# Optimization experiments

Measured on AMD Instinct MI355X. Metric: run time of the kernel, lower is better.

## Reference

```python
import jax, jax.numpy as jnp
import numpy as np

B, C, H, W = 2, 64, 128, 128
KH = KW = 3
K = KH * KW
PAD = 1


def conv(x, w, b, pad):
    out = jax.lax.conv_general_dilated(
        x, w, window_strides=(1, 1), padding=[(pad, pad), (pad, pad)],
        dimension_numbers=("NCHW", "OIHW", "NCHW"))
    return out + b[None, :, None, None]


def leaky_relu(x, slope=0.2):
    return jnp.where(x >= 0, x, slope * x)


def deform_conv(img, offset, mask, w, b):
    # img: [B,C,Hi,Wi]; offset: [B,2K,H,W] (dy,dx interleaved per tap); mask: [B,K,H,W]
    Bb, Ci, Hi, Wi = img.shape
    Ho, Wo = offset.shape[2], offset.shape[3]
    off = offset.reshape(Bb, K, 2, Ho, Wo)
    dy, dx = off[:, :, 0], off[:, :, 1]
    ki, kj = jnp.meshgrid(jnp.arange(KH), jnp.arange(KW), indexing="ij")
    ki = ki.reshape(K).astype(img.dtype)
    kj = kj.reshape(K).astype(img.dtype)
    base_h = (jnp.arange(Ho) - PAD).astype(img.dtype)
    base_w = (jnp.arange(Wo) - PAD).astype(img.dtype)
    ys = base_h[None, None, :, None] + ki[None, :, None, None] + dy  # [B,K,Ho,Wo]
    xs = base_w[None, None, None, :] + kj[None, :, None, None] + dx

    y0 = jnp.floor(ys)
    x0 = jnp.floor(xs)
    ty = ys - y0
    tx = xs - x0
    y0i = y0.astype(jnp.int32)
    x0i = x0.astype(jnp.int32)
    flat = img.reshape(Bb, Ci, Hi * Wi)

    def corner(yi, xi, wgt):
        valid = (yi >= 0) & (yi < Hi) & (xi >= 0) & (xi < Wi)
        yc = jnp.clip(yi, 0, Hi - 1)
        xc = jnp.clip(xi, 0, Wi - 1)
        idx = (yc * Wi + xc).reshape(Bb, 1, -1)
        v = jnp.take_along_axis(flat, jnp.broadcast_to(idx, (Bb, Ci, idx.shape[-1])), axis=2)
        v = v.reshape(Bb, Ci, K, Ho, Wo)
        return v * (wgt * valid.astype(img.dtype))[:, None]

    samp = (corner(y0i, x0i, (1 - ty) * (1 - tx))
            + corner(y0i, x0i + 1, (1 - ty) * tx)
            + corner(y0i + 1, x0i, ty * (1 - tx))
            + corner(y0i + 1, x0i + 1, ty * tx))  # [B,C,K,Ho,Wo]
    out = jnp.einsum("ock,bckhw->bohw", w.reshape(w.shape[0], Ci, K), samp * mask[:, None])
    return out + b[None, :, None, None]


def setup_inputs() -> dict:
    key = jax.random.key(0)
    ks = jax.random.split(key, 8)
    s = 0.05  # keep predicted offsets in a realistic few-pixel range
    return {
        "x": jax.random.normal(ks[0], (B, C, H, W), jnp.float32),
        "y": jax.random.normal(ks[1], (B, C, H, W), jnp.float32),
        "w0": jax.random.normal(ks[2], (C, C, 1, 1), jnp.float32) * s,
        "b0": jnp.zeros((C,), jnp.float32),
        "w_om": jax.random.normal(ks[3], (3 * K, 2 * C, KH, KW), jnp.float32) * s,
        "b_om": jnp.zeros((3 * K,), jnp.float32),
        "w_dc": jax.random.normal(ks[4], (C, C, KH, KW), jnp.float32) * s,
        "b_dc": jnp.zeros((C,), jnp.float32),
        "w1": jax.random.normal(ks[5], (C, C, KH, KW), jnp.float32) * s,
        "b1": jnp.zeros((C,), jnp.float32),
        "w2": jax.random.normal(ks[6], (C, C, KH, KW), jnp.float32) * s,
        "b2": jnp.zeros((C,), jnp.float32),
    }


def reference(x, y, w0, b0, w_om, b_om, w_dc, b_dc, w1, b1, w2, b2):
    x0 = conv(x, w0, b0, pad=0)  # 1x1 projection
    om = conv(jnp.concatenate([x0, y], axis=1), w_om, b_om, pad=PAD)
    offset = om[:, : 2 * K]
    mask = 2.0 * jax.nn.sigmoid(om[:, 2 * K :])
    out = x0 + deform_conv(y, offset, mask, w_dc, b_dc)
    return conv(leaky_relu(conv(out, w1, b1, pad=PAD)), w2, b2, pad=PAD) + out
```

## Files before the change

kernel.cpp:

```cpp
#include <hip/hip_runtime.h>
#include <hip/hip_bf16.h>
#include <math.h>

#define BB 2
#define CCH 64
#define HH 128
#define WWD 128
#define HWv (HH*WWD)
#define KK 9
#define KSTEP 18
#define OMKS 36
#define TCOLS 34
#define CSTR 72
#define CSTR2 136
#define DROW 584

typedef __attribute__((ext_vector_type(8))) short bf16x8;
typedef __attribute__((ext_vector_type(4))) float f32x4;
typedef unsigned short u16;
typedef unsigned int u32;

__device__ inline u16 f2bf(float f) {
  __hip_bfloat16 h = __float2bfloat16(f);
  return *reinterpret_cast<u16*>(&h);
}
__device__ inline u32 f2bf2(float lo, float hi) {
  return ((u32)f2bf(hi) << 16) | (u32)f2bf(lo);
}
__device__ inline float bfLO(u32 v) { return __uint_as_float(v << 16); }
__device__ inline float bfHI(u32 v) { return __uint_as_float(v & 0xffff0000u); }
__device__ inline float bf2f(u16 v) { return __uint_as_float((u32)v << 16); }

__global__ __launch_bounds__(256) void c1y_pack_k(const float* __restrict__ x,
    const float* __restrict__ y, const float* __restrict__ w0,
    const float* __restrict__ b0, const float* __restrict__ w_dc,
    const float* __restrict__ w1, const float* __restrict__ w2,
    const float* __restrict__ w_om, u16* __restrict__ x0bf,
    u16* __restrict__ yt, u16* __restrict__ pk_dc, u16* __restrict__ pk_w1,
    u16* __restrict__ pk_w2, u16* __restrict__ pk_om) {
  #define S1ROW 72
  __shared__ __align__(16) float smem[64 * 65];
  int tid = threadIdx.x;

  if (blockIdx.x >= 512) {
    int blk = blockIdx.x - 512;
    if (blk < 432) {
      const float* w = blk < 144 ? w_dc : (blk < 288 ? w1 : w2);
      u16* dst = blk < 144 ? pk_dc : (blk < 288 ? pk_w1 : pk_w2);
      int idx = (blk % 144) * 256 + tid;
      int j = idx & 7, l = (idx >> 3) & 63;
      int s = (idx >> 9) % 18, q = idx / 9216;
      int co = q * 16 + (l & 15);
      int kp = s * 32 + (l >> 4) * 8 + j;
      dst[idx] = f2bf(w[(co * 64 + (kp & 63)) * 9 + (kp >> 6)]);
    } else {
      int idx = (blk - 432) * 256 + tid;
      int j = idx & 7, l = (idx >> 3) & 63;
      int s = (idx >> 9) % 36, q = idx / 18432;
      int co = q * 16 + (l & 15);
      int kp = s * 32 + (l >> 4) * 8 + j;
      pk_om[idx] = (co < 27)
          ? f2bf(w_om[(co * 128 + (kp & 127)) * 9 + (kp >> 7)]) : (u16)0;
    }
    return;
  }

  u16* samp1 = (u16*)smem;
  int lane = tid & 63, q = tid >> 6;
  int pixbase = blockIdx.x * 64;
  int hwb = pixbase & (HWv - 1);
  int b = pixbase >> 14;
  int co = q * 16 + (lane & 15);
  int g = lane >> 4;

  bf16x8 wfrag[2];
  #pragma unroll
  for (int s = 0; s < 2; s++) {
    const float* wp = w0 + co * 64 + s * 32 + g * 8;
    u16 tw[8];
    #pragma unroll
    for (int j = 0; j < 8; j++) tw[j] = f2bf(wp[j]);
    wfrag[s] = *(bf16x8*)tw;
  }

  {
    const float* src = y + (size_t)b * CCH * HWv;
    #pragma unroll
    for (int i = 0; i < 16; i++) {
      int ci = i * 4 + q;
      smem[ci * 65 + lane] = src[(size_t)ci * HWv + hwb + lane];
    }
    __syncthreads();
    u32* dst32 = (u32*)(yt + ((size_t)b * HWv + hwb) * 64);
    int lane2 = tid & 31, rr = tid >> 5;
    #pragma unroll
    for (int i = 0; i < 8; i++) {
      int row = i * 8 + rr;
      dst32[row * 32 + lane2] = f2bf2(smem[(2 * lane2) * 65 + row],
                                      smem[(2 * lane2 + 1) * 65 + row]);
    }
    __syncthreads();
  }

  {
    u16 tmp[16];
    #pragma unroll
    for (int i = 0; i < 16; i++) {
      int ci = q * 16 + i;
      tmp[i] = f2bf(x[((size_t)b * CCH + ci) * HWv + hwb + lane]);
    }
    #pragma unroll
    for (int i = 0; i < 2; i++)
      *(bf16x8*)(samp1 + lane * S1ROW + q * 16 + i * 8) = *(bf16x8*)(tmp + i * 8);
  }
  __syncthreads();
  f32x4 acc[4] = {{0,0,0,0},{0,0,0,0},{0,0,0,0},{0,0,0,0}};
  #pragma unroll
  for (int s = 0; s < 2; s++) {
    #pragma unroll
    for (int t = 0; t < 4; t++) {
      bf16x8 a = *(const bf16x8*)(samp1 + (t * 16 + (lane & 15)) * S1ROW + g * 8 + s * 32);
      acc[t] = __builtin_amdgcn_mfma_f32_16x16x32_bf16(a, wfrag[s], acc[t], 0, 0, 0);
    }
  }
  float bv = b0[co];
  u16* dst = x0bf + ((size_t)b * HWv + hwb + g * 4) * 64 + co;
  #pragma unroll
  for (int t = 0; t < 4; t++)
    #pragma unroll
    for (int r = 0; r < 4; r++)
      dst[(size_t)(t * 16 + r) * 64] = f2bf(acc[t][r] + bv);
}

__global__ __launch_bounds__(512) void omd_k(const u16* __restrict__ x0bf,
    const u16* __restrict__ yt, const u16* __restrict__ pk_om,
    const u16* __restrict__ pk_dc, const float* __restrict__ b_om,
    const float* __restrict__ b_dc, u16* __restrict__ ob) {
  __shared__ __align__(16) u16 A[18688];
  __shared__ __align__(16) int prm[576][8];
  __shared__ __align__(16) float omv[64 * 28];
  u32* A32 = (u32*)A;
  u32* dsamp32 = (u32*)A;
  u16* dsamp = A;
  int tid = threadIdx.x;
  int lane = tid & 63, q = tid >> 6;
  int blk = (blockIdx.x & 7) * 64 + (blockIdx.x >> 3);
  int wq = blk & 3, rp = (blk >> 2) & 63, b = blk >> 8;
  int h0 = rp * 2, wb = wq * 32;
  const u32* x0b32 = (const u32*)x0bf + (size_t)b * HWv * 32;
  const u32* yt32  = (const u32*)yt + (size_t)b * HWv * 32;

  {
    int lane2 = tid & 31, g16 = tid >> 5;
    int cofs = lane2 * 2;
    const u32* srcb = (lane2 < 16) ? (x0b32 + cofs) : (yt32 + cofs - 32);
    #pragma unroll
    for (int i = 0; i < 9; i++) {
      int u = g16 + 16 * i;
      if (u < 4 * TCOLS) {
        int r = u / TCOLS, c = u % TCOLS;
        int hh = h0 - 1 + r, ww = wb - 1 + c;
        uint2 v = {0u, 0u};
        if ((unsigned)hh < HH && (unsigned)ww < WWD)
          v = *(const uint2*)(srcb + (size_t)(hh * WWD + ww) * 32);
        *(uint2*)(A32 + u * (CSTR2 / 2) + cofs) = v;
      }
    }
  }
  __syncthreads();

  {
    int r = q & 1, cg = (q >> 1) & 1, cohalf = q >> 2;
    f32x4 acc = {0.f, 0.f, 0.f, 0.f};
    const bf16x8* bp = (const bf16x8*)pk_om + (size_t)(cohalf * OMKS) * 64 + lane;
    #pragma unroll
    for (int s = 0; s < OMKS; s++) {
      int kk = s >> 2;
      int addr = ((r + kk / 3) * TCOLS + cg * 16 + (lane & 15) + (kk % 3)) * CSTR2
                 + (s & 3) * 32 + (lane >> 4) * 8;
      bf16x8 a = *(const bf16x8*)(A + addr);
      acc = __builtin_amdgcn_mfma_f32_16x16x32_bf16(a, bp[(size_t)s * 64], acc, 0, 0, 0);
    }
    int co = cohalf * 16 + (lane & 15);
    if (co < 27) {
      float bv = b_om[co];
      int px = r * 32 + cg * 16 + (lane >> 4) * 4;
      #pragma unroll
      for (int j = 0; j < 4; j++)
        omv[(px + j) * 28 + co] = acc[j] + bv;
    }
  }
  __syncthreads();

  #pragma unroll
  for (int t = 0; t < 2; t++) {
    int u = tid + 512 * t;
    if (u < 576) {
      int pl = u / KK, k = u % KK;
      int r2 = pl >> 5, cl = pl & 31;
      const float* omp = omv + pl * 28;
      float dy = omp[2 * k], dx = omp[2 * k + 1];
      float mk = 2.f / (1.f + expf(-omp[18 + k]));
      float ys = (float)(h0 + r2 - 1 + k / 3) + dy;
      float xs = (float)(wb + cl - 1 + k % 3) + dx;
      float y0f = floorf(ys), x0f = floorf(xs);
      float ty = ys - y0f, tx = xs - x0f;
      int yi = (int)y0f, xi = (int)x0f;
      bool y0v = (unsigned)yi < HH, y1v = (unsigned)(yi + 1) < HH;
      bool x0v = (unsigned)xi < WWD, x1v = (unsigned)(xi + 1) < WWD;
      float w00 = (1.f - ty) * (1.f - tx) * mk * ((y0v && x0v) ? 1.f : 0.f);
      float w01 = (1.f - ty) * tx * mk * ((y0v && x1v) ? 1.f : 0.f);
      float w10 = ty * (1.f - tx) * mk * ((y1v && x0v) ? 1.f : 0.f);
      float w11 = ty * tx * mk * ((y1v && x1v) ? 1.f : 0.f);
      int* p = prm[u];
      *(int4*)p = make_int4(min(max(yi, 0), HH - 1) * (WWD * 32),
                            min(max(yi + 1, 0), HH - 1) * (WWD * 32),
                            min(max(xi, 0), WWD - 1) * 32,
                            min(max(xi + 1, 0), WWD - 1) * 32);
      *(int4*)(p + 4) = make_int4(__float_as_int(w00), __float_as_int(w01),
                                  __float_as_int(w10), __float_as_int(w11));
    }
  }
  __syncthreads();

  #pragma unroll
  for (int h2 = 0; h2 < 2; h2++) {
    {
      int lane4 = tid & 15, g16 = tid >> 4;
      const u32* ytb = yt32 + lane4 * 2;
      #pragma unroll
      for (int i = 0; i < 9; i++) {
        int u = g16 + 32 * i;
        int k = u % 9, pix = u / 9;
        const int* pp = prm[h2 * 288 + u];
        int4 pa = *(const int4*)pp;
        int4 pb = *(const int4*)(pp + 4);
        uint2 v00 = *(const uint2*)(ytb + pa.x + pa.z);
        uint2 v01 = *(const uint2*)(ytb + pa.x + pa.w);
        uint2 v10 = *(const uint2*)(ytb + pa.y + pa.z);
        uint2 v11 = *(const uint2*)(ytb + pa.y + pa.w);
        float w00 = __int_as_float(pb.x), w01 = __int_as_float(pb.y);
        float w10 = __int_as_float(pb.z), w11 = __int_as_float(pb.w);
        float a0 = fmaf(bfLO(v00.x), w00, fmaf(bfLO(v01.x), w01,
                   fmaf(bfLO(v10.x), w10, bfLO(v11.x) * w11)));
        float a1 = fmaf(bfHI(v00.x), w00, fmaf(bfHI(v01.x), w01,
                   fmaf(bfHI(v10.x), w10, bfHI(v11.x) * w11)));
        float a2 = fmaf(bfLO(v00.y), w00, fmaf(bfLO(v01.y), w01,
                   fmaf(bfLO(v10.y), w10, bfLO(v11.y) * w11)));
        float a3 = fmaf(bfHI(v00.y), w00, fmaf(bfHI(v01.y), w01,
                   fmaf(bfHI(v10.y), w10, bfHI(v11.y) * w11)));
        uint2 o = {f2bf2(a0, a1), f2bf2(a2, a3)};
        *(uint2*)(dsamp32 + pix * (DROW / 2) + k * 32 + lane4 * 2) = o;
      }
    }
    __syncthreads();
    {
      int qq = q & 3, pxg = q >> 2;
      f32x4 acc = {0.f, 0.f, 0.f, 0.f};
      const u16* arow = dsamp + (pxg * 16 + (lane & 15)) * DROW + (lane >> 4) * 8;
      const bf16x8* bp = (const bf16x8*)pk_dc + (size_t)(qq * KSTEP) * 64 + lane;
      #pragma unroll
      for (int s = 0; s < KSTEP; s++) {
        bf16x8 a = *(const bf16x8*)(arow + s * 32);
        acc = __builtin_amdgcn_mfma_f32_16x16x32_bf16(a, bp[(size_t)s * 64], acc, 0, 0, 0);
      }
      int co = qq * 16 + (lane & 15);
      int px = pxg * 16 + (lane >> 4) * 4;
      float bv = b_dc[co];
      size_t obase = ((size_t)b * HWv + (h0 + h2) * WWD + wb + px) * 64 + co;
      #pragma unroll
      for (int j = 0; j < 4; j++)
        ob[obase + (size_t)j * 64] =
            f2bf(acc[j] + bv + bf2f(x0bf[obase + (size_t)j * 64]));
    }
    if (h2 == 0) __syncthreads();
  }
}

__global__ __launch_bounds__(512) void rconv12_k(const u16* __restrict__ ob,
    const u16* __restrict__ pk_w1, const u16* __restrict__ pk_w2,
    const float* __restrict__ b1, const float* __restrict__ b2,
    float* __restrict__ outp) {
  #define R2COLS 36
  __shared__ __align__(16) u16 stage[6 * R2COLS * CSTR];
  __shared__ __align__(16) u16 zlds[144 * CSTR];
  u32* stage32 = (u32*)stage;
  int tid = threadIdx.x;
  int lane = tid & 63, q = tid >> 6;
  int blk = (blockIdx.x & 7) * 64 + (blockIdx.x >> 3);
  int wq = blk & 3, rp = (blk >> 2) & 63, b = blk >> 8;
  int h0 = rp * 2, wb = wq * 32;

  {
    int lane4 = tid & 15, g16 = tid >> 4;
    const u32* inb = (const u32*)ob + (size_t)b * HWv * 32 + lane4 * 2;
    #pragma unroll
    for (int i = 0; i < 7; i++) {
      int u = g16 + 32 * i;
      if (u < 6 * R2COLS) {
        int r = u / R2COLS, c = u % R2COLS;
        int hh = h0 - 2 + r, ww = wb - 2 + c;
        uint2 v = {0u, 0u};
        if ((unsigned)hh < HH && (unsigned)ww < WWD)
          v = *(const uint2*)(inb + (size_t)(hh * WWD + ww) * 32);
        *(uint2*)(stage32 + u * (CSTR / 2) + lane4 * 2) = v;
      }
    }
  }
  __syncthreads();

  #pragma unroll
  for (int t = 0; t < 5; t++) {
    int task = q + 8 * t;
    if (task < 36) {
      int g = task >> 2, coq = task & 3;
      int p = g * 16 + (lane & 15);
      if (p > 135) p = 135;
      int r1 = p / 34, c1 = p % 34;
      f32x4 acc = {0.f, 0.f, 0.f, 0.f};
      const bf16x8* bp = (const bf16x8*)pk_w1 + (size_t)(coq * KSTEP) * 64 + lane;
      #pragma unroll
      for (int s = 0; s < KSTEP; s++) {
        int kk = s >> 1;
        int addr = ((r1 + kk / 3) * R2COLS + c1 + kk % 3) * CSTR
                   + (s & 1) * 32 + (lane >> 4) * 8;
        bf16x8 a = *(const bf16x8*)(stage + addr);
        acc = __builtin_amdgcn_mfma_f32_16x16x32_bf16(a, bp[(size_t)s * 64], acc, 0, 0, 0);
      }
      int co = coq * 16 + (lane & 15);
      float bv = b1[co];
      int prow = g * 16 + (lane >> 4) * 4;
      #pragma unroll
      for (int j = 0; j < 4; j++) {
        int pp = prow + j;
        int rr = pp / 34, cc = pp % 34;
        bool inimg = ((unsigned)(h0 - 1 + rr) < HH) && ((unsigned)(wb - 1 + cc) < WWD);
        float v = acc[j] + bv;
        v = v >= 0.f ? v : 0.2f * v;
        zlds[pp * CSTR + co] = inimg ? f2bf(v) : (u16)0;
      }
    }
  }
  __syncthreads();

  int r = q & 1, cg = (q >> 1) & 1, copair = q >> 2;
  f32x4 acc2[2] = {{0,0,0,0},{0,0,0,0}};
  const bf16x8* bp2 = (const bf16x8*)pk_w2 + (size_t)(copair * 2 * KSTEP) * 64 + lane;
  #pragma unroll
  for (int s = 0; s < KSTEP; s++) {
    int kk = s >> 1;
    int p = (r + kk / 3) * 34 + cg * 16 + (lane & 15) + (kk % 3);
    int addr = p * CSTR + (s & 1) * 32 + (lane >> 4) * 8;
    bf16x8 a = *(const bf16x8*)(zlds + addr);
    acc2[0] = __builtin_amdgcn_mfma_f32_16x16x32_bf16(a, bp2[(size_t)s * 64], acc2[0], 0, 0, 0);
    acc2[1] = __builtin_amdgcn_mfma_f32_16x16x32_bf16(a, bp2[(size_t)(KSTEP + s) * 64], acc2[1], 0, 0, 0);
  }
  __syncthreads();

  float* ot = (float*)zlds;
  int pxc = cg * 16 + (lane >> 4) * 4;
  #pragma unroll
  for (int t = 0; t < 2; t++) {
    int co = copair * 32 + t * 16 + (lane & 15);
    float bv = b2[co];
    #pragma unroll
    for (int j = 0; j < 4; j++) {
      int c = pxc + j;
      u16 resv = stage[((r + 2) * R2COLS + c + 2) * CSTR + co];
      ot[co * 72 + r * 36 + c] = acc2[t][j] + bv + bf2f(resv);
    }
  }
  __syncthreads();
  int co = tid >> 3, seg = tid & 7;
  int r2 = seg >> 2, c8 = (seg & 3) * 8;
  const float4* src4 = (const float4*)(ot + co * 72 + r2 * 36 + c8);
  float4 v0 = src4[0], v1 = src4[1];
  float* dst = outp + ((size_t)b * CCH + co) * HWv + (h0 + r2) * WWD + wb + c8;
  *(float4*)dst = v0;
  *(float4*)(dst + 4) = v1;
}

extern "C" void kernel_launch(void* const* d_in, const int* in_sizes, int n_in,
                              void* d_out, int out_size, void* d_ws, size_t ws_size,
                              hipStream_t stream) {
  const float* x    = (const float*)d_in[0];
  const float* y    = (const float*)d_in[1];
  const float* w0   = (const float*)d_in[2];
  const float* b0   = (const float*)d_in[3];
  const float* w_om = (const float*)d_in[4];
  const float* b_om = (const float*)d_in[5];
  const float* w_dc = (const float*)d_in[6];
  const float* b_dc = (const float*)d_in[7];
  const float* w1   = (const float*)d_in[8];
  const float* b1   = (const float*)d_in[9];
  const float* w2   = (const float*)d_in[10];
  const float* b2   = (const float*)d_in[11];
  float* out = (float*)d_out;

  const size_t NFULL = (size_t)BB * CCH * HWv;
  const size_t NPACK = 4 * KSTEP * 64 * 8;
  u16* x0bf = (u16*)d_ws;
  u16* ob   = x0bf + NFULL;
  u16* yt   = ob + NFULL;
  u16* pk_dc = yt + NFULL;
  u16* pk_w1 = pk_dc + NPACK;
  u16* pk_w2 = pk_w1 + NPACK;
  u16* pk_om = pk_w2 + NPACK;

  const int NB = (int)((size_t)BB * HWv / 64);

  c1y_pack_k<<<NB + 576, 256, 0, stream>>>(x, y, w0, b0, w_dc, w1, w2, w_om,
                                           x0bf, yt, pk_dc, pk_w1, pk_w2, pk_om);
  omd_k<<<NB, 512, 0, stream>>>(x0bf, yt, pk_om, pk_dc, b_om, b_dc, ob);
  rconv12_k<<<NB, 512, 0, stream>>>(ob, pk_w1, pk_w2, b1, b2, out);
}
```

Baseline: 52.99 us.

## Widen gathers to 16-byte loads, pair MFMA outputs in conv1, swizzle block order

Halo staging in the offset/mask and residual conv kernels, and the bilinear corner gathers, now use 16-byte uint4 loads per thread instead of 8-byte, so fewer threads cover each pixel row and fewer memory instructions are issued. The first 3x3 conv in rconv12 has each wave compute two 16-channel output tiles that share one A-fragment load, which halves LDS reads per MFMA but raises register pressure and leaves some waves idle in the last round. The projection kernel also gets the same XCD-aware block index swizzle that the other kernels already use.

```diff
diff --git a/kernel.cpp b/kernel.cpp
--- a/kernel.cpp
+++ b/kernel.cpp
@@ -67,7 +67,8 @@
 
   u16* samp1 = (u16*)smem;
   int lane = tid & 63, q = tid >> 6;
-  int pixbase = blockIdx.x * 64;
+  int cblk = (blockIdx.x & 7) * 64 + (blockIdx.x >> 3);
+  int pixbase = cblk * 64;
   int hwb = pixbase & (HWv - 1);
   int b = pixbase >> 14;
   int co = q * 16 + (lane & 15);
@@ -151,19 +152,19 @@
   const u32* yt32  = (const u32*)yt + (size_t)b * HWv * 32;
 
   {
-    int lane2 = tid & 31, g16 = tid >> 5;
-    int cofs = lane2 * 2;
-    const u32* srcb = (lane2 < 16) ? (x0b32 + cofs) : (yt32 + cofs - 32);
-    #pragma unroll
-    for (int i = 0; i < 9; i++) {
-      int u = g16 + 16 * i;
+    int lane2 = tid & 15, g16 = tid >> 4;
+    const u32* srcb = (lane2 < 8) ? (x0b32 + lane2 * 4)
+                                  : (yt32 + (lane2 - 8) * 4);
+    #pragma unroll
+    for (int i = 0; i < 5; i++) {
+      int u = g16 + 32 * i;
       if (u < 4 * TCOLS) {
         int r = u / TCOLS, c = u % TCOLS;
         int hh = h0 - 1 + r, ww = wb - 1 + c;
-        uint2 v = {0u, 0u};
+        uint4 v = {0u, 0u, 0u, 0u};
         if ((unsigned)hh < HH && (unsigned)ww < WWD)
-          v = *(const uint2*)(srcb + (size_t)(hh * WWD + ww) * 32);
-        *(uint2*)(A32 + u * (CSTR2 / 2) + cofs) = v;
+          v = *(const uint4*)(srcb + (size_t)(hh * WWD + ww) * 32);
+        *(uint4*)(A32 + u * (CSTR2 / 2) + lane2 * 4) = v;
       }
     }
   }
@@ -226,31 +227,53 @@
   #pragma unroll
   for (int h2 = 0; h2 < 2; h2++) {
     {
-      int lane4 = tid & 15, g16 = tid >> 4;
-      const u32* ytb = yt32 + lane4 * 2;
-      #pragma unroll
-      for (int i = 0; i < 9; i++) {
-        int u = g16 + 32 * i;
-        int k = u % 9, pix = u / 9;
-        const int* pp = prm[h2 * 288 + u];
-        int4 pa = *(const int4*)pp;
-        int4 pb = *(const int4*)(pp + 4);
-        uint2 v00 = *(const uint2*)(ytb + pa.x + pa.z);
-        uint2 v01 = *(const uint2*)(ytb + pa.x + pa.w);
-        uint2 v10 = *(const uint2*)(ytb + pa.y + pa.z);
-        uint2 v11 = *(const uint2*)(ytb + pa.y + pa.w);
-        float w00 = __int_as_float(pb.x), w01 = __int_as_float(pb.y);
-        float w10 = __int_as_float(pb.z), w11 = __int_as_float(pb.w);
-        float a0 = fmaf(bfLO(v00.x), w00, fmaf(bfLO(v01.x), w01,
-                   fmaf(bfLO(v10.x), w10, bfLO(v11.x) * w11)));
-        float a1 = fmaf(bfHI(v00.x), w00, fmaf(bfHI(v01.x), w01,
-                   fmaf(bfHI(v10.x), w10, bfHI(v11.x) * w11)));
-        float a2 = fmaf(bfLO(v00.y), w00, fmaf(bfLO(v01.y), w01,
-                   fmaf(bfLO(v10.y), w10, bfLO(v11.y) * w11)));
-        float a3 = fmaf(bfHI(v00.y), w00, fmaf(bfHI(v01.y), w01,
-                   fmaf(bfHI(v10.y), w10, bfHI(v11.y) * w11)));
-        uint2 o = {f2bf2(a0, a1), f2bf2(a2, a3)};
-        *(uint2*)(dsamp32 + pix * (DROW / 2) + k * 32 + lane4 * 2) = o;
+      int lane4 = tid & 7, g8 = tid >> 3;
+      const u32* ytb = yt32 + lane4 * 4;
+      #pragma unroll
+      for (int i = 0; i < 5; i++) {
+        int u = g8 + 64 * i;
+        if (u < 288) {
+          int k = u % 9, pix = u / 9;
+          const int* pp = prm[h2 * 288 + u];
+          int4 pa = *(const int4*)pp;
+          int4 pb = *(const int4*)(pp + 4);
+          uint4 v00 = *(const uint4*)(ytb + pa.x + pa.z);
+          uint4 v01 = *(const uint4*)(ytb + pa.x + pa.w);
+          uint4 v10 = *(const uint4*)(ytb + pa.y + pa.z);
+          uint4 v11 = *(const uint4*)(ytb + pa.y + pa.w);
+          float w00 = __int_as_float(pb.x), w01 = __int_as_float(pb.y);
+          float w10 = __int_as_float(pb.z), w11 = __int_as_float(pb.w);
+          uint4 o;
+          {
+            float a0 = fmaf(bfLO(v00.x), w00, fmaf(bfLO(v01.x), w01,
+                       fmaf(bfLO(v10.x), w10, bfLO(v11.x) * w11)));
+            float a1 = fmaf(bfHI(v00.x), w00, fmaf(bfHI(v01.x), w01,
+                       fmaf(bfHI(v10.x), w10, bfHI(v11.x) * w11)));
+            o.x = f2bf2(a0, a1);
+          }
+          {
+            float a0 = fmaf(bfLO(v00.y), w00, fmaf(bfLO(v01.y), w01,
+                       fmaf(bfLO(v10.y), w10, bfLO(v11.y) * w11)));
+            float a1 = fmaf(bfHI(v00.y), w00, fmaf(bfHI(v01.y), w01,
+                       fmaf(bfHI(v10.y), w10, bfHI(v11.y) * w11)));
+            o.y = f2bf2(a0, a1);
+          }
+          {
+            float a0 = fmaf(bfLO(v00.z), w00, fmaf(bfLO(v01.z), w01,
+                       fmaf(bfLO(v10.z), w10, bfLO(v11.z) * w11)));
+            float a1 = fmaf(bfHI(v00.z), w00, fmaf(bfHI(v01.z), w01,
+                       fmaf(bfHI(v10.z), w10, bfHI(v11.z) * w11)));
+            o.z = f2bf2(a0, a1);
+          }
+          {
+            float a0 = fmaf(bfLO(v00.w), w00, fmaf(bfLO(v01.w), w01,
+                       fmaf(bfLO(v10.w), w10, bfLO(v11.w) * w11)));
+            float a1 = fmaf(bfHI(v00.w), w00, fmaf(bfHI(v01.w), w01,
+                       fmaf(bfHI(v10.w), w10, bfHI(v11.w) * w11)));
+            o.w = f2bf2(a0, a1);
+          }
+          *(uint4*)(dsamp32 + pix * (DROW / 2) + k * 32 + lane4 * 4) = o;
+        }
       }
     }
     __syncthreads();
@@ -292,52 +315,56 @@
   int h0 = rp * 2, wb = wq * 32;
 
   {
-    int lane4 = tid & 15, g16 = tid >> 4;
-    const u32* inb = (const u32*)ob + (size_t)b * HWv * 32 + lane4 * 2;
-    #pragma unroll
-    for (int i = 0; i < 7; i++) {
-      int u = g16 + 32 * i;
+    int lane4 = tid & 7, g8 = tid >> 3;
+    const u32* inb = (const u32*)ob + (size_t)b * HWv * 32 + lane4 * 4;
+    #pragma unroll
+    for (int i = 0; i < 4; i++) {
+      int u = g8 + 64 * i;
       if (u < 6 * R2COLS) {
         int r = u / R2COLS, c = u % R2COLS;
         int hh = h0 - 2 + r, ww = wb - 2 + c;
-        uint2 v = {0u, 0u};
+        uint4 v = {0u, 0u, 0u, 0u};
         if ((unsigned)hh < HH && (unsigned)ww < WWD)
-          v = *(const uint2*)(inb + (size_t)(hh * WWD + ww) * 32);
-        *(uint2*)(stage32 + u * (CSTR / 2) + lane4 * 2) = v;
-      }
-    }
-  }
-  __syncthreads();
-
-  #pragma unroll
-  for (int t = 0; t < 5; t++) {
+          v = *(const uint4*)(inb + (size_t)(hh * WWD + ww) * 32);
+        *(uint4*)(stage32 + u * (CSTR / 2) + lane4 * 4) = v;
+      }
+    }
+  }
+  __syncthreads();
+
+  #pragma unroll
+  for (int t = 0; t < 3; t++) {
     int task = q + 8 * t;
-    if (task < 36) {
-      int g = task >> 2, coq = task & 3;
+    if (task < 18) {
+      int g = task >> 1, copair = task & 1;
       int p = g * 16 + (lane & 15);
       if (p > 135) p = 135;
       int r1 = p / 34, c1 = p % 34;
-      f32x4 acc = {0.f, 0.f, 0.f, 0.f};
-      const bf16x8* bp = (const bf16x8*)pk_w1 + (size_t)(coq * KSTEP) * 64 + lane;
+      f32x4 acc[2] = {{0,0,0,0},{0,0,0,0}};
+      const bf16x8* bp = (const bf16x8*)pk_w1 + (size_t)(copair * 2 * KSTEP) * 64 + lane;
       #pragma unroll
       for (int s = 0; s < KSTEP; s++) {
         int kk = s >> 1;
         int addr = ((r1 + kk / 3) * R2COLS + c1 + kk % 3) * CSTR
                    + (s & 1) * 32 + (lane >> 4) * 8;
         bf16x8 a = *(const bf16x8*)(stage + addr);
-        acc = __builtin_amdgcn_mfma_f32_16x16x32_bf16(a, bp[(size_t)s * 64], acc, 0, 0, 0);
-      }
-      int co = coq * 16 + (lane & 15);
-      float bv = b1[co];
+        acc[0] = __builtin_amdgcn_mfma_f32_16x16x32_bf16(a, bp[(size_t)s * 64], acc[0], 0, 0, 0);
+        acc[1] = __builtin_amdgcn_mfma_f32_16x16x32_bf16(a, bp[(size_t)(KSTEP + s) * 64], acc[1], 0, 0, 0);
+      }
       int prow = g * 16 + (lane >> 4) * 4;
       #pragma unroll
-      for (int j = 0; j < 4; j++) {
-        int pp = prow + j;
-        int rr = pp / 34, cc = pp % 34;
-        bool inimg = ((unsigned)(h0 - 1 + rr) < HH) && ((unsigned)(wb - 1 + cc) < WWD);
-        float v = acc[j] + bv;
-        v = v >= 0.f ? v : 0.2f * v;
-        zlds[pp * CSTR + co] = inimg ? f2bf(v) : (u16)0;
+      for (int tt = 0; tt < 2; tt++) {
+        int co = copair * 32 + tt * 16 + (lane & 15);
+        float bv = b1[co];
+        #pragma unroll
+        for (int j = 0; j < 4; j++) {
+          int pp = prow + j;
+          int rr = pp / 34, cc = pp % 34;
+          bool inimg = ((unsigned)(h0 - 1 + rr) < HH) && ((unsigned)(wb - 1 + cc) < WWD);
+          float v = acc[tt][j] + bv;
+          v = v >= 0.f ? v : 0.2f * v;
+          zlds[pp * CSTR + co] = inimg ? f2bf(v) : (u16)0;
+        }
       }
     }
   }
```

Result: slower. 55.96 us (+5.6%).
